# Performance work log

Hardware: AMD Instinct MI355X
Metric: run time of the kernel (lower is better)

## Reference

```python
import jax, jax.numpy as jnp
import numpy as np

jax.config.update("jax_enable_x64", True)

P = 2013265921        # NTT-friendly prime (15 * 2^27 + 1), stand-in for BLS12-381 Fr
G_ROOT = 31           # primitive root of P
LOG_N = 21
N = 1 << LOG_N


def _bit_reverse_perm(n):
    logn = n.bit_length() - 1
    idx = np.arange(n, dtype=np.int64)
    rev = np.zeros(n, dtype=np.int64)
    for b in range(logn):
        rev = (rev << 1) | ((idx >> b) & 1)
    return rev


def _pow_arr(base, exps, mod):
    # vectorized modular exponentiation over numpy int64 exponents (host-side, trace-time)
    res = np.ones_like(exps)
    b = np.int64(base % mod)
    e = exps.copy()
    while e.max() > 0:
        res = np.where(e & 1, (res * b) % mod, res)
        b = (b * b) % mod
        e >>= 1
    return res


_REV = _bit_reverse_perm(N)


def intt(x):
    """Inverse NTT over Z_P, radix-2 DIT with bit-reversal. x: [N] int64 in [0,P)."""
    root = pow(G_ROOT, (P - 1) // N, P)
    iroot = pow(root, P - 2, P)
    x = x[_REV]
    length = 2
    while length <= N:
        half = length // 2
        wlen = pow(iroot, N // length, P)
        tw = jnp.asarray(_pow_arr(wlen, np.arange(half, dtype=np.int64), P))  # [half]
        x = x.reshape(-1, length)
        even, odd = x[:, :half], x[:, half:]
        t = (odd * tw) % P                       # products < 2^62, exact in int64
        x = jnp.concatenate([(even + t) % P, (even - t) % P], axis=1).reshape(-1)
        length *= 2
    n_inv = pow(N, P - 2, P)
    return (x * n_inv) % P


def compress4(a, b, c, d, z):
    """zkp.compress: a + z*b + z^2*c + z^3*d  (mod P). z is a Python int challenge."""
    z1 = z % P
    z2 = (z1 * z1) % P
    z3 = (z2 * z1) % P
    return (a + (b * z1) % P + (c * z2) % P + (d * z3) % P) % P


def commit(poly, bases):
    """KZG commitment proxy: MSM reduced to a scalar-weighted sum of SRS bases."""
    scal = poly.astype(jnp.float32) * np.float32(1.0 / P)  # normalize field elems
    return jnp.einsum('n,nc->c', scal, bases)              # [3]


def reference(w_l, w_r, w_o, w_4, table1, table2, table3, table4,
              q_lookup, powers_of_g, zeta):
    # Round 1: wire polynomials via INTT + commitments via MSM
    w_l_poly = intt(w_l)
    w_r_poly = intt(w_r)
    w_o_poly = intt(w_o)
    w_4_poly = intt(w_4)

    # Lookup: compress tables with zeta, build query table f, split sorted multiset
    t_comp = compress4(table1, table2, table3, table4, zeta)
    table_poly = intt(t_comp)
    w_comp = compress4(w_l, w_r, w_o, w_4, zeta)
    f_comp = jnp.where(q_lookup != 0, w_comp, t_comp)      # compute_query_table
    f_poly = intt(f_comp)

    s = jnp.sort(jnp.concatenate([t_comp, f_comp]))        # combine_split
    h_1, h_2 = s[0::2], s[1::2]
    h_1_poly = intt(h_1)
    h_2_poly = intt(h_2)

    polys = jnp.stack([w_l_poly, w_r_poly, w_o_poly, w_4_poly,
                       table_poly, f_poly, h_1_poly, h_2_poly])  # [8, N]
    commits = jnp.stack([commit(p, powers_of_g) for p in polys])  # [8, 3]
    return commits, polys


def setup_inputs() -> dict:
    key = jax.random.key(0)
    ks = jax.random.split(key, 11)
    fe = lambda k: jax.random.randint(k, (N,), 0, P, dtype=jnp.int64)
    return {
        'w_l': fe(ks[0]), 'w_r': fe(ks[1]), 'w_o': fe(ks[2]), 'w_4': fe(ks[3]),
        'table1': fe(ks[4]), 'table2': fe(ks[5]), 'table3': fe(ks[6]), 'table4': fe(ks[7]),
        'q_lookup': jax.random.randint(ks[8], (N,), 0, 2, dtype=jnp.int64),
        'powers_of_g': jax.random.normal(ks[9], (N, 3), dtype=jnp.float32),
        'zeta': 987654321,
    }
```

## Files before the change

kernel.cpp:

```cpp
#include <hip/hip_runtime.h>
#include <stdint.h>

#define PRIME 2013265921u
#define LOGN 21
#define NN (1u << LOGN)

constexpr uint32_t cpow(uint64_t b, uint64_t e) {
    uint64_t r = 1;
    b %= PRIME;
    while (e) {
        if (e & 1ull) r = r * b % PRIME;
        b = b * b % PRIME;
        e >>= 1;
    }
    return (uint32_t)r;
}
constexpr uint32_t cpinv() {
    uint32_t inv = 1;
    for (int i = 0; i < 6; i++) inv *= 2u - PRIME * inv;
    return inv;
}
constexpr uint32_t NPRIME   = (uint32_t)(0u - cpinv());
constexpr uint32_t RMODP    = (uint32_t)((1ull << 32) % PRIME);
constexpr uint32_t ROOT     = cpow(31u, (PRIME - 1) / NN);
constexpr uint32_t IROOT    = cpow(ROOT, PRIME - 2);
constexpr uint32_t IROOT1K  = cpow(IROOT, 1024);
constexpr uint32_t NINV     = cpow(NN, PRIME - 2);
constexpr uint32_t NINV_M   = (uint32_t)((((uint64_t)NINV) << 32) % PRIME);

__device__ __forceinline__ uint32_t addmod(uint32_t a, uint32_t b) {
    uint32_t s = a + b; return (s >= PRIME) ? s - PRIME : s;
}
__device__ __forceinline__ uint32_t submod(uint32_t a, uint32_t b) {
    return (a >= b) ? (a - b) : (a + PRIME - b);
}
__device__ __forceinline__ uint32_t mulmod(uint32_t a, uint32_t b) {
    return (uint32_t)(((uint64_t)a * (uint64_t)b) % PRIME);
}
__device__ __forceinline__ uint32_t montmul(uint32_t a, uint32_t b) {
    uint64_t t = (uint64_t)a * b;
    uint32_t m = (uint32_t)t * NPRIME;
    uint32_t u = (uint32_t)((t + (uint64_t)m * PRIME) >> 32);
    return (u >= PRIME) ? u - PRIME : u;
}
__device__ uint32_t powmod(uint32_t b, uint32_t e) {
    uint32_t r = 1u;
    while (e) {
        if (e & 1u) r = mulmod(r, b);
        b = mulmod(b, b);
        e >>= 1;
    }
    return r;
}
__device__ __forceinline__ uint32_t tomont(uint32_t x) {
    return (uint32_t)((((uint64_t)x) << 32) % PRIME);
}

__global__ void twiddle_ab_kernel(uint32_t* __restrict__ A, uint32_t* __restrict__ B) {
    uint32_t i = blockIdx.x * blockDim.x + threadIdx.x;
    B[i] = tomont(powmod(IROOT, i));
    A[i] = tomont(powmod(IROOT1K, i));
}
__global__ void twiddle_compact_kernel(const uint32_t* __restrict__ A, const uint32_t* __restrict__ B,
                                       uint32_t* __restrict__ WT1, uint32_t* __restrict__ ROWT,
                                       uint32_t* __restrict__ CW) {
    uint32_t i = blockIdx.x * blockDim.x + threadIdx.x;
    if (i < 4096) {
        if (i == 0) WT1[0] = RMODP;
        else {
            uint32_t s = 31u - __clz(i);
            uint32_t j = i ^ (1u << s);
            uint32_t e = j << (20u - s);
            WT1[i] = montmul(A[e >> 10], B[e & 1023u]);
        }
    }
    if (i < 512) {
        if (i == 0) ROWT[0] = RMODP;
        else {
            uint32_t t = 31u - __clz(i);
            uint32_t e = (i - (1u << t)) << (20u - t);
            ROWT[i] = montmul(A[e >> 10], B[e & 1023u]);
        }
    }
    if (i < 36864) {
        uint32_t s = i >> 12, j = i & 4095u;
        uint32_t e = j << (8u - s);
        CW[i] = montmul(A[e >> 10], B[e & 1023u]);
    }
}

__global__ __launch_bounds__(256) void compress_kernel(
        const int* __restrict__ wl, const int* __restrict__ wr,
        const int* __restrict__ wo, const int* __restrict__ w4,
        const int* __restrict__ t1, const int* __restrict__ t2,
        const int* __restrict__ t3, const int* __restrict__ t4,
        const int* __restrict__ q,  const int* __restrict__ zp,
        uint32_t* __restrict__ tcomp, uint32_t* __restrict__ fcomp,
        unsigned int* __restrict__ hist64) {
    __shared__ unsigned int h64[64];
    if (threadIdx.x < 64) h64[threadIdx.x] = 0;
    __syncthreads();
    uint32_t z1 = ((uint32_t)zp[0]) % PRIME;
    uint32_t z2 = mulmod(z1, z1);
    uint32_t z3 = mulmod(z2, z1);
    uint32_t i0 = (blockIdx.x * 256u + threadIdx.x) * 4u;
    int4 a1 = *reinterpret_cast<const int4*>(&t1[i0]);
    int4 a2 = *reinterpret_cast<const int4*>(&t2[i0]);
    int4 a3 = *reinterpret_cast<const int4*>(&t3[i0]);
    int4 a4 = *reinterpret_cast<const int4*>(&t4[i0]);
    int4 b1 = *reinterpret_cast<const int4*>(&wl[i0]);
    int4 b2 = *reinterpret_cast<const int4*>(&wr[i0]);
    int4 b3 = *reinterpret_cast<const int4*>(&wo[i0]);
    int4 b4 = *reinterpret_cast<const int4*>(&w4[i0]);
    int4 qq = *reinterpret_cast<const int4*>(&q[i0]);
    uint4 tv, fv;
    {
        uint32_t t = addmod(addmod((uint32_t)a1.x, mulmod((uint32_t)a2.x, z1)),
                            addmod(mulmod((uint32_t)a3.x, z2), mulmod((uint32_t)a4.x, z3)));
        uint32_t w = addmod(addmod((uint32_t)b1.x, mulmod((uint32_t)b2.x, z1)),
                            addmod(mulmod((uint32_t)b3.x, z2), mulmod((uint32_t)b4.x, z3)));
        tv.x = t; fv.x = (qq.x != 0) ? w : t;
    }
    {
        uint32_t t = addmod(addmod((uint32_t)a1.y, mulmod((uint32_t)a2.y, z1)),
                            addmod(mulmod((uint32_t)a3.y, z2), mulmod((uint32_t)a4.y, z3)));
        uint32_t w = addmod(addmod((uint32_t)b1.y, mulmod((uint32_t)b2.y, z1)),
                            addmod(mulmod((uint32_t)b3.y, z2), mulmod((uint32_t)b4.y, z3)));
        tv.y = t; fv.y = (qq.y != 0) ? w : t;
    }
    {
        uint32_t t = addmod(addmod((uint32_t)a1.z, mulmod((uint32_t)a2.z, z1)),
                            addmod(mulmod((uint32_t)a3.z, z2), mulmod((uint32_t)a4.z, z3)));
        uint32_t w = addmod(addmod((uint32_t)b1.z, mulmod((uint32_t)b2.z, z1)),
                            addmod(mulmod((uint32_t)b3.z, z2), mulmod((uint32_t)b4.z, z3)));
        tv.z = t; fv.z = (qq.z != 0) ? w : t;
    }
    {
        uint32_t t = addmod(addmod((uint32_t)a1.w, mulmod((uint32_t)a2.w, z1)),
                            addmod(mulmod((uint32_t)a3.w, z2), mulmod((uint32_t)a4.w, z3)));
        uint32_t w = addmod(addmod((uint32_t)b1.w, mulmod((uint32_t)b2.w, z1)),
                            addmod(mulmod((uint32_t)b3.w, z2), mulmod((uint32_t)b4.w, z3)));
        tv.w = t; fv.w = (qq.w != 0) ? w : t;
    }
    *reinterpret_cast<uint4*>(&tcomp[i0]) = tv;
    *reinterpret_cast<uint4*>(&fcomp[i0]) = fv;
    atomicAdd(&h64[tv.x >> 25], 1u); atomicAdd(&h64[fv.x >> 25], 1u);
    atomicAdd(&h64[tv.y >> 25], 1u); atomicAdd(&h64[fv.y >> 25], 1u);
    atomicAdd(&h64[tv.z >> 25], 1u); atomicAdd(&h64[fv.z >> 25], 1u);
    atomicAdd(&h64[tv.w >> 25], 1u); atomicAdd(&h64[fv.w >> 25], 1u);
    __syncthreads();
    if (threadIdx.x < 64 && h64[threadIdx.x])
        atomicAdd(&hist64[threadIdx.x], h64[threadIdx.x]);
}

#define NBUCK 8192

__global__ void scan64_kernel(const unsigned int* __restrict__ hist64,
                              unsigned int* __restrict__ cbase, unsigned int* __restrict__ ccursor) {
    if (threadIdx.x == 0) {
        unsigned int run = 0;
        for (int b = 0; b < 64; b++) { cbase[b] = run; ccursor[b] = run; run += hist64[b]; }
        cbase[64] = run;
    }
}

__global__ __launch_bounds__(256) void pass1_kernel(const uint32_t* __restrict__ tcomp,
                                                    const uint32_t* __restrict__ fcomp,
                                                    unsigned int* __restrict__ ccursor,
                                                    uint32_t* __restrict__ barr1) {
    __shared__ uint32_t grp[4096];
    __shared__ unsigned char grpb[4096];
    __shared__ unsigned int cnt[64], pref[64], curs[64], rbase[64];
    uint32_t tid = threadIdx.x;
    const uint32_t* srcp = (blockIdx.x < 512) ? (tcomp + blockIdx.x * 4096)
                                              : (fcomp + (blockIdx.x - 512) * 4096);
    if (tid < 64) cnt[tid] = 0;
    __syncthreads();
    uint4 vv[4];
    #pragma unroll
    for (uint32_t m = 0; m < 4; m++) {
        uint32_t l = (m * 256u + tid) * 4u;
        vv[m] = *reinterpret_cast<const uint4*>(&srcp[l]);
        atomicAdd(&cnt[vv[m].x >> 25], 1u);
        atomicAdd(&cnt[vv[m].y >> 25], 1u);
        atomicAdd(&cnt[vv[m].z >> 25], 1u);
        atomicAdd(&cnt[vv[m].w >> 25], 1u);
    }
    __syncthreads();
    if (tid == 0) {
        unsigned int run = 0;
        for (int b = 0; b < 64; b++) { pref[b] = run; curs[b] = run; run += cnt[b]; }
    }
    __syncthreads();
    if (tid < 64 && cnt[tid]) rbase[tid] = atomicAdd(&ccursor[tid], cnt[tid]);
    #pragma unroll
    for (uint32_t m = 0; m < 4; m++) {
        uint32_t vs[4] = {vv[m].x, vv[m].y, vv[m].z, vv[m].w};
        #pragma unroll
        for (int j = 0; j < 4; j++) {
            uint32_t v = vs[j];
            uint32_t b = v >> 25;
            unsigned int p = atomicAdd(&curs[b], 1u);
            grp[p] = v; grpb[p] = (unsigned char)b;
        }
    }
    __syncthreads();
    for (uint32_t l = tid; l < 4096; l += 256) {
        uint32_t b = grpb[l];
        barr1[rbase[b] + (l - pref[b])] = grp[l];
    }
}

__global__ __launch_bounds__(256) void fine_hist_kernel(const uint32_t* __restrict__ barr1,
                                                        const unsigned int* __restrict__ cbase,
                                                        unsigned int* __restrict__ hist) {
    __shared__ unsigned int cnt[128];
    uint32_t tid = threadIdx.x;
    uint32_t reg = blockIdx.y;
    if (tid < 128) cnt[tid] = 0;
    __syncthreads();
    uint32_t lo = cbase[reg], hi = cbase[reg + 1];
    for (uint32_t i = lo + blockIdx.x * 256 + tid; i < hi; i += gridDim.x * 256)
        atomicAdd(&cnt[(barr1[i] >> 18) & 127u], 1u);
    __syncthreads();
    if (tid < 128 && cnt[tid]) atomicAdd(&hist[reg * 128 + tid], cnt[tid]);
}

__global__ void scan_kernel(const unsigned int* __restrict__ hist,
                            unsigned int* __restrict__ basearr, unsigned int* __restrict__ fcursor) {
    __shared__ unsigned int ls[256];
    int t = threadIdx.x;
    unsigned int local[32];
    unsigned int s = 0;
    for (int k = 0; k < 32; k++) { local[k] = hist[t * 32 + k]; s += local[k]; }
    ls[t] = s;
    __syncthreads();
    for (int off = 1; off < 256; off <<= 1) {
        unsigned int v = (t >= off) ? ls[t - off] : 0u;
        __syncthreads();
        ls[t] += v;
        __syncthreads();
    }
    unsigned int run = ls[t] - s;
    for (int k = 0; k < 32; k++) {
        basearr[t * 32 + k] = run;
        fcursor[t * 32 + k] = run;
        run += local[k];
    }
    if (t == 255) basearr[NBUCK] = run;
}

__global__ __launch_bounds__(256) void pass2_kernel(const uint32_t* __restrict__ barr1,
                                                    const unsigned int* __restrict__ cbase,
                                                    unsigned int* __restrict__ fcursor,
                                                    uint32_t* __restrict__ barr2) {
    __shared__ uint32_t grp[4096];
    __shared__ unsigned char grpb[4096];
    __shared__ unsigned int cnt[128], pref[128], curs[128], rbase[128];
    uint32_t tid = threadIdx.x;
    uint32_t reg = blockIdx.y;
    uint32_t lo = cbase[reg], hi = cbase[reg + 1];
    for (uint32_t start = lo + blockIdx.x * 4096; start < hi; start += gridDim.x * 4096) {
        uint32_t n = min(4096u, hi - start);
        if (tid < 128) cnt[tid] = 0;
        __syncthreads();
        for (uint32_t l = tid; l < n; l += 256)
            atomicAdd(&cnt[(barr1[start + l] >> 18) & 127u], 1u);
        __syncthreads();
        if (tid == 0) {
            unsigned int run = 0;
            for (int b = 0; b < 128; b++) { pref[b] = run; curs[b] = run; run += cnt[b]; }
        }
        __syncthreads();
        if (tid < 128 && cnt[tid]) rbase[tid] = atomicAdd(&fcursor[reg * 128 + tid], cnt[tid]);
        for (uint32_t l = tid; l < n; l += 256) {
            uint32_t v = barr1[start + l];
            uint32_t b = (v >> 18) & 127u;
            unsigned int p = atomicAdd(&curs[b], 1u);
            grp[p] = v; grpb[p] = (unsigned char)b;
        }
        __syncthreads();
        for (uint32_t l = tid; l < n; l += 256) {
            uint32_t b = grpb[l];
            barr2[rbase[b] + (l - pref[b])] = grp[l];
        }
        __syncthreads();
    }
}

__global__ __launch_bounds__(256) void bucket_sort_kernel(const uint32_t* __restrict__ barr,
                                                          const unsigned int* __restrict__ basearr,
                                                          uint32_t* __restrict__ h1, uint32_t* __restrict__ h2) {
    __shared__ uint32_t ord[4096];
    __shared__ unsigned int cnt[256], pref[256], curs[256];
    uint32_t b  = blockIdx.x;
    uint32_t lo = basearr[b], hi = basearr[b + 1];
    uint32_t n  = hi - lo;
    if (n == 0) return;
    if (n > 4096) n = 4096;
    uint32_t tid = threadIdx.x;
    cnt[tid] = 0;
    __syncthreads();
    for (uint32_t i = tid; i < n; i += 256)
        atomicAdd(&cnt[(barr[lo + i] >> 10) & 255u], 1u);
    __syncthreads();
    if (tid == 0) {
        unsigned int run = 0;
        for (int d = 0; d < 256; d++) { pref[d] = run; curs[d] = run; run += cnt[d]; }
    }
    __syncthreads();
    for (uint32_t i = tid; i < n; i += 256) {
        uint32_t v = barr[lo + i];
        uint32_t d = (v >> 10) & 255u;
        unsigned int p = atomicAdd(&curs[d], 1u);
        ord[p] = v;
    }
    __syncthreads();
    for (uint32_t p = tid; p < n; p += 256) {
        uint32_t v = ord[p];
        uint32_t d = (v >> 10) & 255u;
        uint32_t l0 = pref[d], l1 = l0 + cnt[d];
        uint32_t r = 0;
        for (uint32_t qq = l0; qq < l1; qq++) {
            uint32_t u = ord[qq];
            r += (u < v) || (u == v && qq < p);
        }
        uint32_t gp = lo + l0 + r;
        if (gp & 1) h2[gp >> 1] = v; else h1[gp >> 1] = v;
    }
}

struct SrcPtrs { const uint32_t* p[8]; };

__global__ __launch_bounds__(256) void bitrev_kernel(SrcPtrs srcs, uint32_t* __restrict__ dst) {
    __shared__ uint32_t tile[64 * 65];
    uint32_t bb = blockIdx.x;
    uint32_t xcd = bb & 7u, k = bb >> 3;
    uint32_t poly = k >> 6;
    uint32_t m = (k & 63u) + xcd * 64u;
    const uint32_t* src = srcs.p[poly];
    uint32_t* out = dst + (size_t)poly * NN;
    uint32_t rm = __brev(m) >> 23;
    uint32_t tid = threadIdx.x;
    #pragma unroll
    for (uint32_t mm = 0; mm < 4; mm++) {
        uint32_t l = (mm * 256u + tid) * 4u;
        uint32_t u = l >> 6, v = l & 63u;
        uint4 x = *reinterpret_cast<const uint4*>(&src[(u << 15) | (rm << 6) | v]);
        uint32_t base = u * 65u + v;
        tile[base] = x.x; tile[base + 1] = x.y; tile[base + 2] = x.z; tile[base + 3] = x.w;
    }
    __syncthreads();
    #pragma unroll
    for (uint32_t mm = 0; mm < 4; mm++) {
        uint32_t l = (mm * 256u + tid) * 4u;
        uint32_t a = l >> 6, b4 = l & 63u;
        uint32_t ra = __brev(a) >> 26;
        uint4 x;
        x.x = tile[(__brev(b4)     >> 26) * 65u + ra];
        x.y = tile[(__brev(b4 + 1) >> 26) * 65u + ra];
        x.z = tile[(__brev(b4 + 2) >> 26) * 65u + ra];
        x.w = tile[(__brev(b4 + 3) >> 26) * 65u + ra];
        *reinterpret_cast<uint4*>(&out[(a << 15) | (m << 6) | b4]) = x;
    }
}

__device__ __forceinline__ uint32_t padi(uint32_t i) { return i + (i >> 5); }

__global__ __launch_bounds__(256) void ntt_phase1_kernel(uint32_t* __restrict__ polys,
                                                         const uint32_t* __restrict__ WT1) {
    __shared__ uint32_t wt[4096];
    __shared__ uint32_t sd[4224];
    uint32_t bb = blockIdx.x;
    uint32_t xcd = bb & 7u, k = bb >> 3;
    uint32_t poly = k >> 6;
    uint32_t chunk = (k & 63u) + xcd * 64u;
    uint32_t* x = polys + (size_t)poly * NN + (size_t)chunk * 4096;
    #pragma unroll
    for (uint32_t m = 0; m < 4; m++) {
        uint32_t l = m * 1024 + threadIdx.x * 4;
        uint4 v = *reinterpret_cast<const uint4*>(&x[l]);
        uint4 w = *reinterpret_cast<const uint4*>(&WT1[l]);
        uint32_t p = padi(l);
        sd[p] = v.x; sd[p + 1] = v.y; sd[p + 2] = v.z; sd[p + 3] = v.w;
        *reinterpret_cast<uint4*>(&wt[l]) = w;
    }
    __syncthreads();
    #pragma unroll
    for (int t = 0; t < 6; t++) {
        uint32_t h = 1u << (2 * t);
        #pragma unroll
        for (uint32_t m = 0; m < 4; m++) {
            uint32_t q = threadIdx.x + (m << 8);
            uint32_t j = q & (h - 1);
            uint32_t grp = q >> (2 * t);
            uint32_t i0 = (grp << (2 * t + 2)) + j;
            uint32_t w1  = wt[h + j];
            uint32_t w2  = wt[2 * h + j];
            uint32_t w2j = wt[3 * h + j];
            uint32_t p0 = padi(i0), p1 = padi(i0 + h), p2 = padi(i0 + 2 * h), p3 = padi(i0 + 3 * h);
            uint32_t a0 = sd[p0], a1 = sd[p1], a2 = sd[p2], a3 = sd[p3];
            uint32_t t1 = montmul(w1, a1), t3 = montmul(w1, a3);
            uint32_t b0 = addmod(a0, t1), b1 = submod(a0, t1);
            uint32_t b2 = addmod(a2, t3), b3 = submod(a2, t3);
            uint32_t u2 = montmul(w2, b2), u3 = montmul(w2j, b3);
            sd[p0] = addmod(b0, u2);
            sd[p2] = submod(b0, u2);
            sd[p1] = addmod(b1, u3);
            sd[p3] = submod(b1, u3);
        }
        __syncthreads();
    }
    #pragma unroll
    for (uint32_t m = 0; m < 4; m++) {
        uint32_t l = m * 1024 + threadIdx.x * 4;
        uint32_t p = padi(l);
        uint4 v;
        v.x = montmul(sd[p], NINV_M);
        v.y = montmul(sd[p + 1], NINV_M);
        v.z = montmul(sd[p + 2], NINV_M);
        v.w = montmul(sd[p + 3], NINV_M);
        *reinterpret_cast<uint4*>(&x[l]) = v;
    }
}

__global__ __launch_bounds__(512) void ntt_phase2_kernel(uint32_t* __restrict__ polys,
                                                         const uint32_t* __restrict__ ROWT,
                                                         const uint32_t* __restrict__ CW,
                                                         const float* __restrict__ g,
                                                         double* __restrict__ partials) {
    __shared__ __align__(16) uint32_t sd[16384];
    uint32_t b = blockIdx.x;
    uint32_t xcd = b & 7u, k = b >> 3;
    uint32_t poly = k >> 4;
    uint32_t c0_idx = xcd * 16u + (k & 15u);
    uint32_t* x = polys + (size_t)poly * NN;
    uint32_t c0 = c0_idx * 32u;
    uint32_t tid = threadIdx.x;
    uint32_t c = tid & 31u;
    uint32_t rt = tid >> 5;
    uint32_t cg = tid & 7u;
    uint32_t r0 = tid >> 3;

    #pragma unroll
    for (uint32_t kk = 0; kk < 8; kk++) {
        uint32_t row = r0 + kk * 64;
        uint4 v = *reinterpret_cast<const uint4*>(&x[(row << 12) + c0 + 4 * cg]);
        *reinterpret_cast<uint4*>(&sd[row * 32 + 4 * cg]) = v;
    }
    uint32_t cw[9];
    #pragma unroll
    for (int s = 0; s < 9; s++) cw[s] = CW[s * 4096 + c0 + c];
    __syncthreads();

    #pragma unroll
    for (int s = 0; s < 8; s += 2) {
        uint32_t h = 1u << s;
        #pragma unroll
        for (uint32_t m = 0; m < 8; m++) {
            uint32_t u = (rt << 3) + m;
            uint32_t kk = u & (h - 1);
            uint32_t grp = u >> s;
            uint32_t r = (grp << (s + 2)) + kk;
            uint32_t w1  = montmul(ROWT[h + kk], cw[s]);
            uint32_t w2  = montmul(ROWT[2 * h + kk], cw[s + 1]);
            uint32_t w2j = montmul(ROWT[3 * h + kk], cw[s + 1]);
            uint32_t i0 = (r << 5) + c;
            uint32_t i1 = ((r + h) << 5) + c;
            uint32_t i2 = ((r + 2 * h) << 5) + c;
            uint32_t i3 = ((r + 3 * h) << 5) + c;
            uint32_t a0 = sd[i0], a1 = sd[i1], a2 = sd[i2], a3 = sd[i3];
            uint32_t t1 = montmul(w1, a1), t3 = montmul(w1, a3);
            uint32_t b0 = addmod(a0, t1), b1 = submod(a0, t1);
            uint32_t b2 = addmod(a2, t3), b3 = submod(a2, t3);
            uint32_t u2 = montmul(w2, b2), u3 = montmul(w2j, b3);
            sd[i0] = addmod(b0, u2);
            sd[i2] = submod(b0, u2);
            sd[i1] = addmod(b1, u3);
            sd[i3] = submod(b1, u3);
        }
        __syncthreads();
    }
    #pragma unroll
    for (uint32_t m = 0; m < 16; m++) {
        uint32_t kk = (rt << 4) + m;
        uint32_t w = montmul(ROWT[256 + kk], cw[8]);
        uint32_t i0 = (kk << 5) + c, i1 = ((kk + 256) << 5) + c;
        uint32_t u = sd[i0];
        uint32_t v = montmul(sd[i1], w);
        sd[i0] = addmod(u, v);
        sd[i1] = submod(u, v);
    }
    __syncthreads();

    float* xf = (float*)x;
    const float invp = (float)(1.0 / 2013265921.0);
    double a0 = 0.0, a1 = 0.0, a2 = 0.0;
    #pragma unroll
    for (uint32_t kk = 0; kk < 8; kk++) {
        uint32_t row = r0 + kk * 64;
        uint32_t idx0 = (row << 12) + c0 + 4 * cg;
        uint32_t base = row * 32 + 4 * cg;
        float f0 = (float)sd[base], f1 = (float)sd[base + 1];
        float f2 = (float)sd[base + 2], f3 = (float)sd[base + 3];
        float4 fv = make_float4(f0, f1, f2, f3);
        *reinterpret_cast<float4*>(&xf[idx0]) = fv;
        const float4* gp = reinterpret_cast<const float4*>(&g[(size_t)idx0 * 3]);
        float4 g0 = gp[0], g1 = gp[1], g2 = gp[2];
        float s0 = f0 * invp, s1 = f1 * invp, s2 = f2 * invp, s3 = f3 * invp;
        a0 += (double)(s0 * g0.x) + (double)(s1 * g0.w) + (double)(s2 * g1.z) + (double)(s3 * g2.y);
        a1 += (double)(s0 * g0.y) + (double)(s1 * g1.x) + (double)(s2 * g1.w) + (double)(s3 * g2.z);
        a2 += (double)(s0 * g0.z) + (double)(s1 * g1.y) + (double)(s2 * g2.x) + (double)(s3 * g2.w);
    }
    __syncthreads();
    double* red = (double*)sd;
    double v3[3] = {a0, a1, a2};
    #pragma unroll
    for (int kq = 0; kq < 3; kq++) {
        red[tid] = v3[kq];
        __syncthreads();
        for (int off = 256; off > 0; off >>= 1) {
            if (tid < off) red[tid] += red[tid + off];
            __syncthreads();
        }
        if (tid == 0) partials[((size_t)poly * 128 + c0_idx) * 3 + kq] = red[0];
        __syncthreads();
    }
}

__global__ void reduce_commits_kernel(const double* __restrict__ partials, float* __restrict__ outf) {
    __shared__ double red[256];
    int t = threadIdx.x;
    for (int k = 0; k < 24; k++) {
        int p = k / 3, cc = k % 3;
        red[t] = (t < 128) ? partials[((size_t)p * 128 + t) * 3 + cc] : 0.0;
        __syncthreads();
        for (int off = 128; off > 0; off >>= 1) {
            if (t < off) red[t] += red[t + off];
            __syncthreads();
        }
        if (t == 0) outf[k] = (float)red[0];
        __syncthreads();
    }
}

extern "C" void kernel_launch(void* const* d_in, const int* in_sizes, int n_in,
                              void* d_out, int out_size, void* d_ws, size_t ws_size,
                              hipStream_t stream) {
    const int* wl = (const int*)d_in[0];
    const int* wr = (const int*)d_in[1];
    const int* wo = (const int*)d_in[2];
    const int* w4 = (const int*)d_in[3];
    const int* t1 = (const int*)d_in[4];
    const int* t2 = (const int*)d_in[5];
    const int* t3 = (const int*)d_in[6];
    const int* t4 = (const int*)d_in[7];
    const int* q  = (const int*)d_in[8];
    const float* g = (const float*)d_in[9];
    const int* zp = (const int*)d_in[10];

    char* ws = (char*)d_ws;
    uint32_t* WT1  = (uint32_t*)(ws);
    uint32_t* ROWT = (uint32_t*)(ws + (64u  << 10));
    uint32_t* CW   = (uint32_t*)(ws + (128u << 10));
    uint32_t* tcomp  = (uint32_t*)(ws + (8ull  << 20));
    uint32_t* fcomp  = (uint32_t*)(ws + (16ull << 20));
    uint32_t* h1     = (uint32_t*)(ws + (24ull << 20));
    uint32_t* h2     = (uint32_t*)(ws + (32ull << 20));
    unsigned int* hist    = (unsigned int*)(ws + (40ull << 20));
    unsigned int* basearr = (unsigned int*)(ws + (40ull << 20) + (64u  << 10));
    unsigned int* fcursor = (unsigned int*)(ws + (40ull << 20) + (128u << 10));
    uint32_t*     tA      = (uint32_t*)   (ws + (40ull << 20) + (200u << 10));
    uint32_t*     tB      = (uint32_t*)   (ws + (40ull << 20) + (208u << 10));
    unsigned int* hist64  = (unsigned int*)(ws + (40ull << 20) + (216u << 10));
    unsigned int* cbase   = (unsigned int*)(ws + (40ull << 20) + (224u << 10));
    unsigned int* ccursor = (unsigned int*)(ws + (40ull << 20) + (232u << 10));
    double*       partials = (double*)    (ws + (40ull << 20) + (256u << 10));

    float* outf = (float*)d_out;
    uint32_t* outpolys = (uint32_t*)outf + 24;
    uint32_t* barr1 = (uint32_t*)outf + 1024;
    uint32_t* barr2 = (uint32_t*)outf + 1024 + (5u << 20);

    hipMemsetAsync(hist, 0, NBUCK * sizeof(unsigned int), stream);
    hipMemsetAsync(hist64, 0, 64 * sizeof(unsigned int), stream);

    twiddle_ab_kernel<<<4, 256, 0, stream>>>(tA, tB);
    twiddle_compact_kernel<<<144, 256, 0, stream>>>(tA, tB, WT1, ROWT, CW);

    compress_kernel<<<2048, 256, 0, stream>>>(wl, wr, wo, w4, t1, t2, t3, t4, q, zp,
                                              tcomp, fcomp, hist64);
    scan64_kernel<<<1, 64, 0, stream>>>(hist64, cbase, ccursor);
    pass1_kernel<<<1024, 256, 0, stream>>>(tcomp, fcomp, ccursor, barr1);
    fine_hist_kernel<<<dim3(16, 64), 256, 0, stream>>>(barr1, cbase, hist);
    scan_kernel<<<1, 256, 0, stream>>>(hist, basearr, fcursor);
    pass2_kernel<<<dim3(16, 64), 256, 0, stream>>>(barr1, cbase, fcursor, barr2);
    bucket_sort_kernel<<<NBUCK, 256, 0, stream>>>(barr2, basearr, h1, h2);

    SrcPtrs sp;
    sp.p[0] = (const uint32_t*)wl;
    sp.p[1] = (const uint32_t*)wr;
    sp.p[2] = (const uint32_t*)wo;
    sp.p[3] = (const uint32_t*)w4;
    sp.p[4] = tcomp;
    sp.p[5] = fcomp;
    sp.p[6] = h1;
    sp.p[7] = h2;
    bitrev_kernel<<<4096, 256, 0, stream>>>(sp, outpolys);
    ntt_phase1_kernel<<<4096, 256, 0, stream>>>(outpolys, WT1);
    ntt_phase2_kernel<<<1024, 512, 0, stream>>>(outpolys, ROWT, CW, g, partials);

    reduce_commits_kernel<<<1, 256, 0, stream>>>(partials, outf);
}
```

Baseline: 326.8 us.

## Fuse bit-reversal permutation into NTT phase-1 load and merge twiddle kernels

The separate bit-reversal transpose kernel is removed. NTT phase 1 now gathers its 4096-element chunk directly from the source polynomials with strided scalar loads, writing them into shared memory at bit-reversed positions. This drops one full read and write pass over 8 polynomials of 2^21 elements, but the gather uses a 512-element stride and is no longer vectorised, which can hurt coalescing. The two twiddle kernels are also merged into one that computes each twiddle by direct powmod instead of going through two lookup tables, which adds per-thread compute to save a launch.

After: 340.1 us. 1.04x slower.

```diff
diff --git a/kernel.cpp b/kernel.cpp
--- a/kernel.cpp
+++ b/kernel.cpp
@@ -24,7 +24,6 @@
 constexpr uint32_t RMODP    = (uint32_t)((1ull << 32) % PRIME);
 constexpr uint32_t ROOT     = cpow(31u, (PRIME - 1) / NN);
 constexpr uint32_t IROOT    = cpow(ROOT, PRIME - 2);
-constexpr uint32_t IROOT1K  = cpow(IROOT, 1024);
 constexpr uint32_t NINV     = cpow(NN, PRIME - 2);
 constexpr uint32_t NINV_M   = (uint32_t)((((uint64_t)NINV) << 32) % PRIME);
 
@@ -56,36 +55,27 @@
     return (uint32_t)((((uint64_t)x) << 32) % PRIME);
 }
 
-__global__ void twiddle_ab_kernel(uint32_t* __restrict__ A, uint32_t* __restrict__ B) {
-    uint32_t i = blockIdx.x * blockDim.x + threadIdx.x;
-    B[i] = tomont(powmod(IROOT, i));
-    A[i] = tomont(powmod(IROOT1K, i));
-}
-__global__ void twiddle_compact_kernel(const uint32_t* __restrict__ A, const uint32_t* __restrict__ B,
-                                       uint32_t* __restrict__ WT1, uint32_t* __restrict__ ROWT,
-                                       uint32_t* __restrict__ CW) {
+__global__ void twiddle_all_kernel(uint32_t* __restrict__ WT1, uint32_t* __restrict__ ROWT,
+                                   uint32_t* __restrict__ CW) {
     uint32_t i = blockIdx.x * blockDim.x + threadIdx.x;
     if (i < 4096) {
         if (i == 0) WT1[0] = RMODP;
         else {
             uint32_t s = 31u - __clz(i);
             uint32_t j = i ^ (1u << s);
-            uint32_t e = j << (20u - s);
-            WT1[i] = montmul(A[e >> 10], B[e & 1023u]);
+            WT1[i] = tomont(powmod(IROOT, j << (20u - s)));
         }
     }
     if (i < 512) {
         if (i == 0) ROWT[0] = RMODP;
         else {
             uint32_t t = 31u - __clz(i);
-            uint32_t e = (i - (1u << t)) << (20u - t);
-            ROWT[i] = montmul(A[e >> 10], B[e & 1023u]);
+            ROWT[i] = tomont(powmod(IROOT, (i - (1u << t)) << (20u - t)));
         }
     }
     if (i < 36864) {
         uint32_t s = i >> 12, j = i & 4095u;
-        uint32_t e = j << (8u - s);
-        CW[i] = montmul(A[e >> 10], B[e & 1023u]);
+        CW[i] = tomont(powmod(IROOT, j << (8u - s)));
     }
 }
 
@@ -332,66 +322,39 @@
 
 struct SrcPtrs { const uint32_t* p[8]; };
 
-__global__ __launch_bounds__(256) void bitrev_kernel(SrcPtrs srcs, uint32_t* __restrict__ dst) {
-    __shared__ uint32_t tile[64 * 65];
-    uint32_t bb = blockIdx.x;
-    uint32_t xcd = bb & 7u, k = bb >> 3;
-    uint32_t poly = k >> 6;
-    uint32_t m = (k & 63u) + xcd * 64u;
-    const uint32_t* src = srcs.p[poly];
-    uint32_t* out = dst + (size_t)poly * NN;
-    uint32_t rm = __brev(m) >> 23;
-    uint32_t tid = threadIdx.x;
-    #pragma unroll
-    for (uint32_t mm = 0; mm < 4; mm++) {
-        uint32_t l = (mm * 256u + tid) * 4u;
-        uint32_t u = l >> 6, v = l & 63u;
-        uint4 x = *reinterpret_cast<const uint4*>(&src[(u << 15) | (rm << 6) | v]);
-        uint32_t base = u * 65u + v;
-        tile[base] = x.x; tile[base + 1] = x.y; tile[base + 2] = x.z; tile[base + 3] = x.w;
-    }
-    __syncthreads();
-    #pragma unroll
-    for (uint32_t mm = 0; mm < 4; mm++) {
-        uint32_t l = (mm * 256u + tid) * 4u;
-        uint32_t a = l >> 6, b4 = l & 63u;
-        uint32_t ra = __brev(a) >> 26;
-        uint4 x;
-        x.x = tile[(__brev(b4)     >> 26) * 65u + ra];
-        x.y = tile[(__brev(b4 + 1) >> 26) * 65u + ra];
-        x.z = tile[(__brev(b4 + 2) >> 26) * 65u + ra];
-        x.w = tile[(__brev(b4 + 3) >> 26) * 65u + ra];
-        *reinterpret_cast<uint4*>(&out[(a << 15) | (m << 6) | b4]) = x;
-    }
-}
-
 __device__ __forceinline__ uint32_t padi(uint32_t i) { return i + (i >> 5); }
 
-__global__ __launch_bounds__(256) void ntt_phase1_kernel(uint32_t* __restrict__ polys,
+__global__ __launch_bounds__(256) void ntt_phase1_kernel(SrcPtrs srcs, uint32_t* __restrict__ polys,
                                                          const uint32_t* __restrict__ WT1) {
     __shared__ uint32_t wt[4096];
     __shared__ uint32_t sd[4224];
     uint32_t bb = blockIdx.x;
     uint32_t xcd = bb & 7u, k = bb >> 3;
     uint32_t poly = k >> 6;
-    uint32_t chunk = (k & 63u) + xcd * 64u;
+    uint32_t r = xcd * 64u + (k & 63u);
+    uint32_t chunk = __brev(r) >> 23;
+    const uint32_t* src = srcs.p[poly];
     uint32_t* x = polys + (size_t)poly * NN + (size_t)chunk * 4096;
+    uint32_t tid = threadIdx.x;
+
     #pragma unroll
     for (uint32_t m = 0; m < 4; m++) {
-        uint32_t l = m * 1024 + threadIdx.x * 4;
-        uint4 v = *reinterpret_cast<const uint4*>(&x[l]);
-        uint4 w = *reinterpret_cast<const uint4*>(&WT1[l]);
-        uint32_t p = padi(l);
-        sd[p] = v.x; sd[p + 1] = v.y; sd[p + 2] = v.z; sd[p + 3] = v.w;
-        *reinterpret_cast<uint4*>(&wt[l]) = w;
-    }
-    __syncthreads();
+        uint32_t l = m * 1024 + tid * 4;
+        *reinterpret_cast<uint4*>(&wt[l]) = *reinterpret_cast<const uint4*>(&WT1[l]);
+    }
+    #pragma unroll
+    for (uint32_t it = 0; it < 16; it++) {
+        uint32_t m = tid + it * 256u;
+        sd[padi(__brev(m) >> 20)] = src[m * 512u + r];
+    }
+    __syncthreads();
+
     #pragma unroll
     for (int t = 0; t < 6; t++) {
         uint32_t h = 1u << (2 * t);
         #pragma unroll
         for (uint32_t m = 0; m < 4; m++) {
-            uint32_t q = threadIdx.x + (m << 8);
+            uint32_t q = tid + (m << 8);
             uint32_t j = q & (h - 1);
             uint32_t grp = q >> (2 * t);
             uint32_t i0 = (grp << (2 * t + 2)) + j;
@@ -413,7 +376,7 @@
     }
     #pragma unroll
     for (uint32_t m = 0; m < 4; m++) {
-        uint32_t l = m * 1024 + threadIdx.x * 4;
+        uint32_t l = m * 1024 + tid * 4;
         uint32_t p = padi(l);
         uint4 v;
         v.x = montmul(sd[p], NINV_M);
@@ -570,8 +533,6 @@
     unsigned int* hist    = (unsigned int*)(ws + (40ull << 20));
     unsigned int* basearr = (unsigned int*)(ws + (40ull << 20) + (64u  << 10));
     unsigned int* fcursor = (unsigned int*)(ws + (40ull << 20) + (128u << 10));
-    uint32_t*     tA      = (uint32_t*)   (ws + (40ull << 20) + (200u << 10));
-    uint32_t*     tB      = (uint32_t*)   (ws + (40ull << 20) + (208u << 10));
     unsigned int* hist64  = (unsigned int*)(ws + (40ull << 20) + (216u << 10));
     unsigned int* cbase   = (unsigned int*)(ws + (40ull << 20) + (224u << 10));
     unsigned int* ccursor = (unsigned int*)(ws + (40ull << 20) + (232u << 10));
@@ -585,8 +546,7 @@
     hipMemsetAsync(hist, 0, NBUCK * sizeof(unsigned int), stream);
     hipMemsetAsync(hist64, 0, 64 * sizeof(unsigned int), stream);
 
-    twiddle_ab_kernel<<<4, 256, 0, stream>>>(tA, tB);
-    twiddle_compact_kernel<<<144, 256, 0, stream>>>(tA, tB, WT1, ROWT, CW);
+    twiddle_all_kernel<<<144, 256, 0, stream>>>(WT1, ROWT, CW);
 
     compress_kernel<<<2048, 256, 0, stream>>>(wl, wr, wo, w4, t1, t2, t3, t4, q, zp,
                                               tcomp, fcomp, hist64);
@@ -606,8 +566,7 @@
     sp.p[5] = fcomp;
     sp.p[6] = h1;
     sp.p[7] = h2;
-    bitrev_kernel<<<4096, 256, 0, stream>>>(sp, outpolys);
-    ntt_phase1_kernel<<<4096, 256, 0, stream>>>(outpolys, WT1);
+    ntt_phase1_kernel<<<4096, 256, 0, stream>>>(sp, outpolys, WT1);
     ntt_phase2_kernel<<<1024, 512, 0, stream>>>(outpolys, ROWT, CW, g, partials);
 
     reduce_commits_kernel<<<1, 256, 0, stream>>>(partials, outf);
```
